# Kernel tuning notes

Hardware: AMD Instinct MI355X
Metric: run time of the kernel (lower is better)

The kernel has to match this reference:

```python
import jax, jax.numpy as jnp
import numpy as np

N_COMP = 8
N_BASIS = 16
N_FEATURES = 64
N_CAT = 8
N_CONT = 56
N_UNIQUE = 100
BATCH = 32768
T0, T1 = 0.0, 10.0
SEP = 1e-3  # constants.MIN_TRANSITION_POINT_SEP
SIGNS = np.array([1.0, -1.0, 1.0, -1.0, 1.0, -1.0, 1.0, -1.0], dtype=np.float32)
CONT_IDX = np.arange(N_CONT)
CAT_IDX = np.arange(N_CONT, N_FEATURES)


def _offset():
    # torch_inverse_softplus(avg_interval_per_feature)
    v = (T1 - T0) / N_COMP / (N_FEATURES + 1)
    return float(np.log(np.exp(v) - 1.0))


def setup_inputs():
    key = jax.random.key(0)
    ks = jax.random.split(key, 11)
    off = _offset()
    B = jax.random.normal(ks[0], (BATCH, N_CONT, N_BASIS), jnp.float32)
    codes = jax.random.randint(ks[1], (BATCH, N_CAT), 0, N_UNIQUE)
    B_cat = jax.nn.one_hot(codes, N_UNIQUE, dtype=jnp.float32).reshape(BATCH, N_CAT * N_UNIQUE)
    Wh = jax.random.normal(ks[2], (N_BASIS, N_CONT, N_COMP), jnp.float32) + off
    Wh_cat = jax.random.normal(ks[3], (N_CAT, N_UNIQUE, N_COMP), jnp.float32) + off
    bh = jax.random.normal(ks[4], (N_COMP,), jnp.float32) + off
    Wv = jax.random.normal(ks[5], (N_BASIS, N_CONT, N_COMP), jnp.float32)
    Wv_cat = jax.random.normal(ks[6], (N_CAT, N_UNIQUE, N_COMP), jnp.float32)
    bv = jax.random.normal(ks[7], (N_COMP,), jnp.float32)
    Wic = jax.random.normal(ks[8], (N_BASIS, N_CONT, 1), jnp.float32)
    Wic_cat = jax.random.normal(ks[9], (N_CAT, N_UNIQUE, 1), jnp.float32)
    bic = jax.random.normal(ks[10], (1,), jnp.float32)
    return {"B": B, "B_cat": B_cat, "Wh": Wh, "Wh_cat": Wh_cat, "bh": bh,
            "Wv": Wv, "Wv_cat": Wv_cat, "bv": bv,
            "Wic": Wic, "Wic_cat": Wic_cat, "bic": bic}


def _calculate_gams(B, B_cat, W, W_cat, bias, positive):
    # continuous: per-feature small matmul  (b,i,k) x (k,i,c) -> (b,c,i)
    cont = jnp.einsum('bik,kic->bci', B, W)
    # categorical: one-hot gather expressed as blockwise matmul  (b,f,n) x (f,n,c) -> (b,c,f)
    cat = jnp.einsum('bfn,fnc->bcf', B_cat.reshape(B.shape[0], N_CAT, N_UNIQUE), W_cat)
    c = W.shape[2]
    out = jnp.zeros((B.shape[0], c, N_FEATURES + 1), dtype=B.dtype)
    out = out.at[:, :, CONT_IDX].set(cont)
    out = out.at[:, :, CAT_IDX].set(cat)
    out = out.at[:, :, -1].set(bias[None, :])
    return jax.nn.softplus(out) if positive else out


def reference(B, B_cat, Wh, Wh_cat, bh, Wv, Wv_cat, bv, Wic, Wic_cat, bic):
    H = _calculate_gams(B, B_cat, Wh, Wh_cat, bh, True)      # (b, n_comp, n_feat+1)
    V = _calculate_gams(B, B_cat, Wv, Wv_cat, bv, True)      # (b, n_comp, n_feat+1)
    IC = _calculate_gams(B, B_cat, Wic, Wic_cat, bic, False)  # (b, 1, n_feat+1)
    b = B.shape[0]
    signs = jnp.asarray(SIGNS)
    h_sum = H.sum(-1)   # (b, n_comp) per-segment horizontal increments
    v_sum = V.sum(-1)
    sep = SEP * jnp.arange(1, N_COMP + 1, dtype=B.dtype)
    # sequential cumulative build == prefix sums over the composition axis
    t = jnp.concatenate([jnp.full((b, 1), T0, B.dtype),
                         T0 + jnp.cumsum(h_sum, axis=1) + sep], axis=1)  # (b, n_comp+1)
    x0 = IC.sum(-1)     # (b, 1)
    x = jnp.concatenate([x0, x0 + jnp.cumsum(signs * v_sum, axis=1)], axis=1)
    # bounded composition: clamp the last horizontal coordinate
    t = t.at[:, -1].set(jnp.maximum(t[:, -2] + SEP, T1))
    return jnp.stack([t, x], axis=-1)  # (b, n_comp+1, 2)
```

## Files before the change

### kernel.cpp

```cpp
#include <hip/hip_runtime.h>

#define NCOMP 8
#define NCONT 56
#define NCAT 8
#define NU 100
#define SEPC 1e-3f
#define T1F 10.0f

#define FSTRIDE 35
#define WS_NW4 2048
#define WS_BIAS_OFF 32768

typedef __fp16 f16x2 __attribute__((ext_vector_type(2)));
typedef _Float16 h2arith __attribute__((ext_vector_type(2)));

union H8 { f16x2 h2[4]; float4 f4; };

__device__ __forceinline__ float sp(float x) {
    return 0.69314718f * __builtin_amdgcn_logf(1.0f + __builtin_amdgcn_exp2f(x * 1.44269504f));
}

__device__ __forceinline__ f16x2 pkrtz(float a, float b) {
    return __builtin_amdgcn_cvt_pkrtz(a, b);
}

__device__ __forceinline__ float fdot2(f16x2 a, f16x2 b, float c) {
    return __builtin_amdgcn_fdot2(a, b, c, false);
}

__device__ __forceinline__ h2arith h2shfl_xor(h2arith v, int off) {
    int i = __builtin_bit_cast(int, v);
    i = __shfl_xor(i, off, 64);
    return __builtin_bit_cast(h2arith, i);
}

__device__ __forceinline__ void acc_cont(const float4* __restrict__ pw,
                                         float4 a0, float4 a1, float4 a2, float4 a3,
                                         float* sh, float* sw, float& ic) {
    f16x2 ba[8];
    ba[0] = pkrtz(a0.x, a0.y); ba[1] = pkrtz(a0.z, a0.w);
    ba[2] = pkrtz(a1.x, a1.y); ba[3] = pkrtz(a1.z, a1.w);
    ba[4] = pkrtz(a2.x, a2.y); ba[5] = pkrtz(a2.z, a2.w);
    ba[6] = pkrtz(a3.x, a3.y); ba[7] = pkrtz(a3.z, a3.w);
#pragma unroll
    for (int c = 0; c < NCOMP; ++c) {
        H8 u0, u1, v0, v1;
        u0.f4 = pw[2 * c];      u1.f4 = pw[2 * c + 1];
        v0.f4 = pw[16 + 2 * c]; v1.f4 = pw[17 + 2 * c];
        float hA = 0.0f, vA = 0.0f;
#pragma unroll
        for (int p = 0; p < 4; ++p) {
            hA = fdot2(ba[p], u0.h2[p], hA);
            vA = fdot2(ba[p], v0.h2[p], vA);
        }
#pragma unroll
        for (int p = 0; p < 4; ++p) {
            hA = fdot2(ba[4 + p], u1.h2[p], hA);
            vA = fdot2(ba[4 + p], v1.h2[p], vA);
        }
        sh[c] += sp(hA);
        sw[c] += sp(vA);
    }
    H8 i0, i1;
    i0.f4 = pw[32]; i1.f4 = pw[33];
    float iA = 0.0f;
#pragma unroll
    for (int p = 0; p < 4; ++p) iA = fdot2(ba[p], i0.h2[p], iA);
#pragma unroll
    for (int p = 0; p < 4; ++p) iA = fdot2(ba[4 + p], i1.h2[p], iA);
    ic += iA;
}

__global__ __launch_bounds__(512) void prep_kernel(
    const float* __restrict__ Wh, const float* __restrict__ Wv,
    const float* __restrict__ Wic, const float* __restrict__ bh,
    const float* __restrict__ bv, const float* __restrict__ bic,
    float4* __restrict__ ws)
{
    const int id = blockIdx.x * 512 + threadIdx.x;
    const int i  = id / FSTRIDE;
    const int rr = id - i * FSTRIDE;
    H8 u;
    u.f4 = make_float4(0.f, 0.f, 0.f, 0.f);
    if (i < NCONT && rr < 34) {
        if (rr < 32) {
            const int c = (rr & 15) >> 1;
            const int t = rr & 1;
            const float* W  = (rr < 16) ? Wh : Wv;
            const float* gp = W + (size_t)(8 * t) * 448 + i * 8 + c;
#pragma unroll
            for (int p = 0; p < 4; ++p)
                u.h2[p] = pkrtz(gp[(2 * p) * 448], gp[(2 * p + 1) * 448]);
        } else {
            const int t = rr - 32;
            const float* gp = Wic + (size_t)(8 * t) * 56 + i;
#pragma unroll
            for (int p = 0; p < 4; ++p)
                u.h2[p] = pkrtz(gp[(2 * p) * 56], gp[(2 * p + 1) * 56]);
        }
    }
    ws[id] = u.f4;
    if (id < NCOMP) {
        float2* b2 = (float2*)((char*)ws + WS_BIAS_OFF);
        b2[id] = make_float2(sp(bh[id]), sp(bv[id]));
    }
    if (id == NCOMP) {
        *((float*)((char*)ws + WS_BIAS_OFF + 64)) = bic[0];
    }
}

__global__ __launch_bounds__(512, 4) void tpm_kernel(
    const float* __restrict__ B, const float* __restrict__ Bcat,
    const float* __restrict__ Whc, const float* __restrict__ Wvc,
    const float* __restrict__ Wicc, const float4* __restrict__ ws,
    float* __restrict__ out)
{
    __shared__ float4 sW[WS_NW4];
    __shared__ float2 sBias[NCOMP];
    __shared__ float  sBic;
    __shared__ int    sCode[8][4][NCAT];

    const int tid  = threadIdx.x;
    const int lane = tid & 63;
    const int widx = tid >> 6;
    const int s = lane & 15;
    const int g = lane >> 4;
    const int R0 = (((blockIdx.x << 3) + widx) << 2);
    const int r = R0 + g;
    const float* browp = B + (size_t)r * 896;

    float4 cb0, cb1, cb2, cb3;
    {
        const float4* p = (const float4*)(browp + s * 16);
        cb0 = p[0]; cb1 = p[1]; cb2 = p[2]; cb3 = p[3];
    }

#pragma unroll
    for (int k = 0; k < 4; ++k) sW[tid + k * 512] = ws[tid + k * 512];
    if (tid < NCOMP) sBias[tid] = ((const float2*)((const char*)ws + WS_BIAS_OFF))[tid];
    if (tid == NCOMP) sBic = *((const float*)((const char*)ws + WS_BIAS_OFF + 64));
    __syncthreads();

    {
        const float4* pc = (const float4*)(Bcat + (size_t)R0 * 800);
#pragma unroll
        for (int it = 0; it < 13; ++it) {
            int idx = it * 64 + lane;
            if (it < 12 || idx < 800) {
                int row = idx / 200;
                int pos = idx - row * 200;
                float4 q = pc[idx];
                float n = (float)(4 * pos);
                float sc = q.x * (n + 1.0f) + q.y * (n + 2.0f) + q.z * (n + 3.0f) + q.w * (n + 4.0f);
                if (sc > 0.5f) {
                    int p = (int)sc - 1;
                    int f = p / NU;
                    sCode[widx][row][f] = p - f * NU;
                }
            }
        }
    }
    __threadfence_block();

    float4 p3a, p3b, p3c, p3d;
    float p3ic = 0.0f;
    if (s >= 8) {
        int fi = s - 8;
        int cc = sCode[widx][g][fi];
        int gA = fi * NU + cc;
        const float4* qh = (const float4*)(Whc + gA * 8);
        const float4* qv = (const float4*)(Wvc + gA * 8);
        p3a = qh[0]; p3b = qh[1]; p3c = qv[0]; p3d = qv[1];
        p3ic = Wicc[gA];
    }

    float sh[NCOMP], sw[NCOMP];
    float ic = 0.0f;
#pragma unroll
    for (int c = 0; c < NCOMP; ++c) { sh[c] = sw[c] = 0.0f; }

#pragma unroll
    for (int j = 0; j < 3; ++j) {
        float4 nb0, nb1, nb2, nb3;
        if (j < 2) {
            const float4* p = (const float4*)(browp + (s + 16 * (j + 1)) * 16);
            nb0 = p[0]; nb1 = p[1]; nb2 = p[2]; nb3 = p[3];
        } else {
            int f3 = (s < 8) ? (s + 48) : 48;
            const float4* p = (const float4*)(browp + f3 * 16);
            nb0 = p[0]; nb1 = p[1]; nb2 = p[2]; nb3 = p[3];
        }
        acc_cont(sW + (s + 16 * j) * FSTRIDE, cb0, cb1, cb2, cb3, sh, sw, ic);
        cb0 = nb0; cb1 = nb1; cb2 = nb2; cb3 = nb3;
    }

    if (s < 8) {
        acc_cont(sW + (s + 48) * FSTRIDE, cb0, cb1, cb2, cb3, sh, sw, ic);
    } else {
        sh[0] += sp(p3a.x); sh[1] += sp(p3a.y); sh[2] += sp(p3a.z); sh[3] += sp(p3a.w);
        sh[4] += sp(p3b.x); sh[5] += sp(p3b.y); sh[6] += sp(p3b.z); sh[7] += sp(p3b.w);
        sw[0] += sp(p3c.x); sw[1] += sp(p3c.y); sw[2] += sp(p3c.z); sw[3] += sp(p3c.w);
        sw[4] += sp(p3d.x); sw[5] += sp(p3d.y); sw[6] += sp(p3d.z); sw[7] += sp(p3d.w);
        ic += p3ic;
    }

    h2arith hw[NCOMP];
#pragma unroll
    for (int c = 0; c < NCOMP; ++c)
        hw[c] = __builtin_bit_cast(h2arith, pkrtz(sh[c], sw[c]));
#pragma unroll
    for (int off = 8; off >= 1; off >>= 1) {
#pragma unroll
        for (int c = 0; c < NCOMP; ++c)
            hw[c] = hw[c] + h2shfl_xor(hw[c], off);
        ic += __shfl_xor(ic, off, 64);
    }

    if (s < 9) {
        int m = (s == 8) ? 7 : s;
        float tj = SEPC * (float)s;
        float xj = ic + sBic;
#pragma unroll
        for (int c = 0; c < NCOMP; ++c) {
            float2 bb2 = sBias[c];
            if (c < m) tj += (float)hw[c][0] + bb2.x;
            if (c < s) {
                float vv = (float)hw[c][1] + bb2.y;
                xj += (c & 1) ? -vv : vv;
            }
        }
        if (s == 8) tj = fmaxf(tj, T1F);
        float2 o; o.x = tj; o.y = xj;
        ((float2*)out)[(size_t)r * 9 + s] = o;
    }
}

extern "C" void kernel_launch(void* const* d_in, const int* in_sizes, int n_in,
                              void* d_out, int out_size, void* d_ws, size_t ws_size,
                              hipStream_t stream) {
    (void)in_sizes; (void)n_in; (void)out_size; (void)ws_size;
    const float* B    = (const float*)d_in[0];
    const float* Bcat = (const float*)d_in[1];
    const float* Wh   = (const float*)d_in[2];
    const float* Whc  = (const float*)d_in[3];
    const float* bh   = (const float*)d_in[4];
    const float* Wv   = (const float*)d_in[5];
    const float* Wvc  = (const float*)d_in[6];
    const float* bv   = (const float*)d_in[7];
    const float* Wic  = (const float*)d_in[8];
    const float* Wicc = (const float*)d_in[9];
    const float* bic  = (const float*)d_in[10];
    float* out = (float*)d_out;
    float4* ws = (float4*)d_ws;

    hipLaunchKernelGGL(prep_kernel, dim3(4), dim3(512), 0, stream,
                       Wh, Wv, Wic, bh, bv, bic, ws);
    hipLaunchKernelGGL(tpm_kernel, dim3(1024), dim3(512), 0, stream,
                       B, Bcat, Whc, Wvc, Wicc, ws, out);
}
```

Measured before the change: 260.3 us.

## Read packed weights directly from global memory instead of staging in LDS

Drops the per-block copy of the 32KB packed fp16 weight table into shared memory and its barrier. The weights are re-laid out feature-major (row r, feature f) so that lanes of a wave reading consecutive features make coalesced global/L2 loads. With LDS use down to the tiny code table, the launch bound's occupancy hint is raised from 4 to 8. The cost is that every block repeatedly reads weights through the cache hierarchy instead of LDS, with higher latency per access.

Result: slower. 326.6 us (+25.4%).

```diff
diff --git a/kernel.cpp b/kernel.cpp
--- a/kernel.cpp
+++ b/kernel.cpp
@@ -7,9 +7,7 @@
 #define SEPC 1e-3f
 #define T1F 10.0f
 
-#define FSTRIDE 35
-#define WS_NW4 2048
-#define WS_BIAS_OFF 32768
+#define WS_BIAS_OFF 31744
 
 typedef __fp16 f16x2 __attribute__((ext_vector_type(2)));
 typedef _Float16 h2arith __attribute__((ext_vector_type(2)));
@@ -34,7 +32,7 @@
     return __builtin_bit_cast(h2arith, i);
 }
 
-__device__ __forceinline__ void acc_cont(const float4* __restrict__ pw,
+__device__ __forceinline__ void acc_cont(const float4* __restrict__ pwf,
                                          float4 a0, float4 a1, float4 a2, float4 a3,
                                          float* sh, float* sw, float& ic) {
     f16x2 ba[8];
@@ -45,8 +43,8 @@
 #pragma unroll
     for (int c = 0; c < NCOMP; ++c) {
         H8 u0, u1, v0, v1;
-        u0.f4 = pw[2 * c];      u1.f4 = pw[2 * c + 1];
-        v0.f4 = pw[16 + 2 * c]; v1.f4 = pw[17 + 2 * c];
+        u0.f4 = pwf[(2 * c) * NCONT];      u1.f4 = pwf[(2 * c + 1) * NCONT];
+        v0.f4 = pwf[(16 + 2 * c) * NCONT]; v1.f4 = pwf[(17 + 2 * c) * NCONT];
         float hA = 0.0f, vA = 0.0f;
 #pragma unroll
         for (int p = 0; p < 4; ++p) {
@@ -62,7 +60,7 @@
         sw[c] += sp(vA);
     }
     H8 i0, i1;
-    i0.f4 = pw[32]; i1.f4 = pw[33];
+    i0.f4 = pwf[32 * NCONT]; i1.f4 = pwf[33 * NCONT];
     float iA = 0.0f;
 #pragma unroll
     for (int p = 0; p < 4; ++p) iA = fdot2(ba[p], i0.h2[p], iA);
@@ -78,28 +76,28 @@
     float4* __restrict__ ws)
 {
     const int id = blockIdx.x * 512 + threadIdx.x;
-    const int i  = id / FSTRIDE;
-    const int rr = id - i * FSTRIDE;
-    H8 u;
-    u.f4 = make_float4(0.f, 0.f, 0.f, 0.f);
-    if (i < NCONT && rr < 34) {
-        if (rr < 32) {
-            const int c = (rr & 15) >> 1;
+    if (id < 34 * NCONT) {
+        const int r = id / NCONT;
+        const int f = id - r * NCONT;
+        H8 u;
+        if (r < 32) {
+            const int rr = r & 15;
+            const int c = rr >> 1;
             const int t = rr & 1;
-            const float* W  = (rr < 16) ? Wh : Wv;
-            const float* gp = W + (size_t)(8 * t) * 448 + i * 8 + c;
+            const float* W  = (r < 16) ? Wh : Wv;
+            const float* gp = W + (size_t)(8 * t) * 448 + f * 8 + c;
 #pragma unroll
             for (int p = 0; p < 4; ++p)
                 u.h2[p] = pkrtz(gp[(2 * p) * 448], gp[(2 * p + 1) * 448]);
         } else {
-            const int t = rr - 32;
-            const float* gp = Wic + (size_t)(8 * t) * 56 + i;
+            const int t = r - 32;
+            const float* gp = Wic + (size_t)(8 * t) * 56 + f;
 #pragma unroll
             for (int p = 0; p < 4; ++p)
                 u.h2[p] = pkrtz(gp[(2 * p) * 56], gp[(2 * p + 1) * 56]);
         }
-    }
-    ws[id] = u.f4;
+        ws[id] = u.f4;
+    }
     if (id < NCOMP) {
         float2* b2 = (float2*)((char*)ws + WS_BIAS_OFF);
         b2[id] = make_float2(sp(bh[id]), sp(bv[id]));
@@ -109,16 +107,13 @@
     }
 }
 
-__global__ __launch_bounds__(512, 4) void tpm_kernel(
+__global__ __launch_bounds__(512, 8) void tpm_kernel(
     const float* __restrict__ B, const float* __restrict__ Bcat,
     const float* __restrict__ Whc, const float* __restrict__ Wvc,
     const float* __restrict__ Wicc, const float4* __restrict__ ws,
     float* __restrict__ out)
 {
-    __shared__ float4 sW[WS_NW4];
-    __shared__ float2 sBias[NCOMP];
-    __shared__ float  sBic;
-    __shared__ int    sCode[8][4][NCAT];
+    __shared__ int sCode[8][4][NCAT];
 
     const int tid  = threadIdx.x;
     const int lane = tid & 63;
@@ -134,12 +129,6 @@
         const float4* p = (const float4*)(browp + s * 16);
         cb0 = p[0]; cb1 = p[1]; cb2 = p[2]; cb3 = p[3];
     }
-
-#pragma unroll
-    for (int k = 0; k < 4; ++k) sW[tid + k * 512] = ws[tid + k * 512];
-    if (tid < NCOMP) sBias[tid] = ((const float2*)((const char*)ws + WS_BIAS_OFF))[tid];
-    if (tid == NCOMP) sBic = *((const float*)((const char*)ws + WS_BIAS_OFF + 64));
-    __syncthreads();
 
     {
         const float4* pc = (const float4*)(Bcat + (size_t)R0 * 800);
@@ -190,12 +179,12 @@
             const float4* p = (const float4*)(browp + f3 * 16);
             nb0 = p[0]; nb1 = p[1]; nb2 = p[2]; nb3 = p[3];
         }
-        acc_cont(sW + (s + 16 * j) * FSTRIDE, cb0, cb1, cb2, cb3, sh, sw, ic);
+        acc_cont(ws + (s + 16 * j), cb0, cb1, cb2, cb3, sh, sw, ic);
         cb0 = nb0; cb1 = nb1; cb2 = nb2; cb3 = nb3;
     }
 
     if (s < 8) {
-        acc_cont(sW + (s + 48) * FSTRIDE, cb0, cb1, cb2, cb3, sh, sw, ic);
+        acc_cont(ws + (s + 48), cb0, cb1, cb2, cb3, sh, sw, ic);
     } else {
         sh[0] += sp(p3a.x); sh[1] += sp(p3a.y); sh[2] += sp(p3a.z); sh[3] += sp(p3a.w);
         sh[4] += sp(p3b.x); sh[5] += sp(p3b.y); sh[6] += sp(p3b.z); sh[7] += sp(p3b.w);
@@ -217,12 +206,14 @@
     }
 
     if (s < 9) {
+        const float2* b2 = (const float2*)((const char*)ws + WS_BIAS_OFF);
+        float bicv = *((const float*)((const char*)ws + WS_BIAS_OFF + 64));
         int m = (s == 8) ? 7 : s;
         float tj = SEPC * (float)s;
-        float xj = ic + sBic;
+        float xj = ic + bicv;
 #pragma unroll
         for (int c = 0; c < NCOMP; ++c) {
-            float2 bb2 = sBias[c];
+            float2 bb2 = b2[c];
             if (c < m) tj += (float)hw[c][0] + bb2.x;
             if (c < s) {
                 float vv = (float)hw[c][1] + bb2.y;
```

## Interleave one-hot categorical scan with continuous accumulation to overlap loads

Applied to the files above, without the earlier changes.

Splits the B_cat one-hot scan into batches of prefetched float4 loads and interleaves them with the three continuous-feature accumulation stages. Previously the whole categorical scan ran, with its own load latency, before any continuous work started. The B_cat reads now overlap with the B reads and the FMA work, at the cost of more live registers. The categorical gather is delayed until after the accumulation.

After: 594.6 us. 2.28x slower.

```diff
diff --git a/kernel.cpp b/kernel.cpp
--- a/kernel.cpp
+++ b/kernel.cpp
@@ -128,12 +128,17 @@
     const int R0 = (((blockIdx.x << 3) + widx) << 2);
     const int r = R0 + g;
     const float* browp = B + (size_t)r * 896;
+    const float4* pcat = (const float4*)(Bcat + (size_t)R0 * 800);
 
     float4 cb0, cb1, cb2, cb3;
     {
         const float4* p = (const float4*)(browp + s * 16);
         cb0 = p[0]; cb1 = p[1]; cb2 = p[2]; cb3 = p[3];
     }
+    float4 qa0 = pcat[lane];
+    float4 qa1 = pcat[64 + lane];
+    float4 qa2 = pcat[128 + lane];
+    float4 qa3 = pcat[192 + lane];
 
 #pragma unroll
     for (int k = 0; k < 4; ++k) sW[tid + k * 512] = ws[tid + k * 512];
@@ -141,25 +146,60 @@
     if (tid == NCOMP) sBic = *((const float*)((const char*)ws + WS_BIAS_OFF + 64));
     __syncthreads();
 
-    {
-        const float4* pc = (const float4*)(Bcat + (size_t)R0 * 800);
-#pragma unroll
-        for (int it = 0; it < 13; ++it) {
-            int idx = it * 64 + lane;
-            if (it < 12 || idx < 800) {
-                int row = idx / 200;
-                int pos = idx - row * 200;
-                float4 q = pc[idx];
-                float n = (float)(4 * pos);
-                float sc = q.x * (n + 1.0f) + q.y * (n + 2.0f) + q.z * (n + 3.0f) + q.w * (n + 4.0f);
-                if (sc > 0.5f) {
-                    int p = (int)sc - 1;
-                    int f = p / NU;
-                    sCode[widx][row][f] = p - f * NU;
-                }
+    auto scan1 = [&](float4 q, int it) {
+        int idx = it * 64 + lane;
+        if (it < 12 || idx < 800) {
+            int row = idx / 200;
+            int pos = idx - row * 200;
+            float n = (float)(4 * pos);
+            float sc = q.x * (n + 1.0f) + q.y * (n + 2.0f) + q.z * (n + 3.0f) + q.w * (n + 4.0f);
+            if (sc > 0.5f) {
+                int p = (int)sc - 1;
+                int f = p / NU;
+                sCode[widx][row][f] = p - f * NU;
             }
         }
-    }
+    };
+
+    float sh[NCOMP], sw[NCOMP];
+    float ic = 0.0f;
+#pragma unroll
+    for (int c = 0; c < NCOMP; ++c) { sh[c] = sw[c] = 0.0f; }
+
+    float4 nb0, nb1, nb2, nb3;
+    {
+        const float4* p = (const float4*)(browp + (s + 16) * 16);
+        nb0 = p[0]; nb1 = p[1]; nb2 = p[2]; nb3 = p[3];
+    }
+    acc_cont(sW + s * FSTRIDE, cb0, cb1, cb2, cb3, sh, sw, ic);
+    scan1(qa0, 0); scan1(qa1, 1); scan1(qa2, 2); scan1(qa3, 3);
+    qa0 = pcat[256 + lane];
+    qa1 = pcat[320 + lane];
+    qa2 = pcat[384 + lane];
+    qa3 = pcat[448 + lane];
+    float4 qa4 = pcat[512 + lane];
+    cb0 = nb0; cb1 = nb1; cb2 = nb2; cb3 = nb3;
+
+    {
+        const float4* p = (const float4*)(browp + (s + 32) * 16);
+        nb0 = p[0]; nb1 = p[1]; nb2 = p[2]; nb3 = p[3];
+    }
+    acc_cont(sW + (s + 16) * FSTRIDE, cb0, cb1, cb2, cb3, sh, sw, ic);
+    scan1(qa0, 4); scan1(qa1, 5); scan1(qa2, 6); scan1(qa3, 7); scan1(qa4, 8);
+    qa0 = pcat[576 + lane];
+    qa1 = pcat[640 + lane];
+    qa2 = pcat[704 + lane];
+    qa3 = make_float4(0.f, 0.f, 0.f, 0.f);
+    if (lane < 32) qa3 = pcat[768 + lane];
+    cb0 = nb0; cb1 = nb1; cb2 = nb2; cb3 = nb3;
+
+    {
+        int f3 = (s < 8) ? (s + 48) : 48;
+        const float4* p = (const float4*)(browp + f3 * 16);
+        nb0 = p[0]; nb1 = p[1]; nb2 = p[2]; nb3 = p[3];
+    }
+    acc_cont(sW + (s + 32) * FSTRIDE, cb0, cb1, cb2, cb3, sh, sw, ic);
+    scan1(qa0, 9); scan1(qa1, 10); scan1(qa2, 11); scan1(qa3, 12);
     __threadfence_block();
 
     float4 p3a, p3b, p3c, p3d;
@@ -173,26 +213,7 @@
         p3a = qh[0]; p3b = qh[1]; p3c = qv[0]; p3d = qv[1];
         p3ic = Wicc[gA];
     }
-
-    float sh[NCOMP], sw[NCOMP];
-    float ic = 0.0f;
-#pragma unroll
-    for (int c = 0; c < NCOMP; ++c) { sh[c] = sw[c] = 0.0f; }
-
-#pragma unroll
-    for (int j = 0; j < 3; ++j) {
-        float4 nb0, nb1, nb2, nb3;
-        if (j < 2) {
-            const float4* p = (const float4*)(browp + (s + 16 * (j + 1)) * 16);
-            nb0 = p[0]; nb1 = p[1]; nb2 = p[2]; nb3 = p[3];
-        } else {
-            int f3 = (s < 8) ? (s + 48) : 48;
-            const float4* p = (const float4*)(browp + f3 * 16);
-            nb0 = p[0]; nb1 = p[1]; nb2 = p[2]; nb3 = p[3];
-        }
-        acc_cont(sW + (s + 16 * j) * FSTRIDE, cb0, cb1, cb2, cb3, sh, sw, ic);
-        cb0 = nb0; cb1 = nb1; cb2 = nb2; cb3 = nb3;
-    }
+    cb0 = nb0; cb1 = nb1; cb2 = nb2; cb3 = nb3;
 
     if (s < 8) {
         acc_cont(sW + (s + 48) * FSTRIDE, cb0, cb1, cb2, cb3, sh, sw, ic);
```

## Split one-hot categorical scan into a separate kernel writing byte codes

Applied to the files above, without the earlier changes.

Moves the scan of the one-hot categorical matrix out of the main kernel into a dedicated scan_kernel that writes per-row byte codes to workspace. The main kernel then reads those codes directly, drops its shared-memory code table, and moves the shared weight staging and barrier after the categorical gathers. The intent is to shorten the main kernel's critical path and let it run with less memory traffic interleaved with the B stream. It adds an extra kernel launch and a small round trip through global memory for the codes, while the total bytes read from Bcat stay the same.

After: 265.5 us. About the same (+2.0%).

```diff
diff --git a/kernel.cpp b/kernel.cpp
--- a/kernel.cpp
+++ b/kernel.cpp
@@ -10,6 +10,7 @@
 #define FSTRIDE 35
 #define WS_NW4 2048
 #define WS_BIAS_OFF 32768
+#define WS_CODES_OFF 65536
 
 typedef __fp16 f16x2 __attribute__((ext_vector_type(2)));
 typedef _Float16 h2arith __attribute__((ext_vector_type(2)));
@@ -109,16 +110,39 @@
     }
 }
 
+__global__ __launch_bounds__(256, 4) void scan_kernel(
+    const float* __restrict__ Bcat, unsigned char* __restrict__ codes)
+{
+    const int t   = blockIdx.x * 256 + threadIdx.x;
+    const int row = t >> 4;
+    const int sub = t & 15;
+    const float4* pc = (const float4*)(Bcat + (size_t)row * 800);
+#pragma unroll
+    for (int k = 0; k < 13; ++k) {
+        int pos = sub + (k << 4);
+        if (pos < 200) {
+            float4 q = pc[pos];
+            float n = (float)(4 * pos);
+            float sc = q.x * (n + 1.0f) + q.y * (n + 2.0f)
+                     + q.z * (n + 3.0f) + q.w * (n + 4.0f);
+            if (sc > 0.5f) {
+                int p = (int)sc - 1;
+                int f = p / NU;
+                codes[(row << 3) + f] = (unsigned char)(p - f * NU);
+            }
+        }
+    }
+}
+
 __global__ __launch_bounds__(512, 4) void tpm_kernel(
-    const float* __restrict__ B, const float* __restrict__ Bcat,
-    const float* __restrict__ Whc, const float* __restrict__ Wvc,
-    const float* __restrict__ Wicc, const float4* __restrict__ ws,
+    const float* __restrict__ B, const float* __restrict__ Whc,
+    const float* __restrict__ Wvc, const float* __restrict__ Wicc,
+    const float4* __restrict__ ws, const unsigned char* __restrict__ codes,
     float* __restrict__ out)
 {
     __shared__ float4 sW[WS_NW4];
     __shared__ float2 sBias[NCOMP];
     __shared__ float  sBic;
-    __shared__ int    sCode[8][4][NCAT];
 
     const int tid  = threadIdx.x;
     const int lane = tid & 63;
@@ -135,44 +159,23 @@
         cb0 = p[0]; cb1 = p[1]; cb2 = p[2]; cb3 = p[3];
     }
 
-#pragma unroll
-    for (int k = 0; k < 4; ++k) sW[tid + k * 512] = ws[tid + k * 512];
-    if (tid < NCOMP) sBias[tid] = ((const float2*)((const char*)ws + WS_BIAS_OFF))[tid];
-    if (tid == NCOMP) sBic = *((const float*)((const char*)ws + WS_BIAS_OFF + 64));
-    __syncthreads();
-
-    {
-        const float4* pc = (const float4*)(Bcat + (size_t)R0 * 800);
-#pragma unroll
-        for (int it = 0; it < 13; ++it) {
-            int idx = it * 64 + lane;
-            if (it < 12 || idx < 800) {
-                int row = idx / 200;
-                int pos = idx - row * 200;
-                float4 q = pc[idx];
-                float n = (float)(4 * pos);
-                float sc = q.x * (n + 1.0f) + q.y * (n + 2.0f) + q.z * (n + 3.0f) + q.w * (n + 4.0f);
-                if (sc > 0.5f) {
-                    int p = (int)sc - 1;
-                    int f = p / NU;
-                    sCode[widx][row][f] = p - f * NU;
-                }
-            }
-        }
-    }
-    __threadfence_block();
-
     float4 p3a, p3b, p3c, p3d;
     float p3ic = 0.0f;
     if (s >= 8) {
         int fi = s - 8;
-        int cc = sCode[widx][g][fi];
+        int cc = codes[(r << 3) + fi];
         int gA = fi * NU + cc;
         const float4* qh = (const float4*)(Whc + gA * 8);
         const float4* qv = (const float4*)(Wvc + gA * 8);
         p3a = qh[0]; p3b = qh[1]; p3c = qv[0]; p3d = qv[1];
         p3ic = Wicc[gA];
     }
+
+#pragma unroll
+    for (int k = 0; k < 4; ++k) sW[tid + k * 512] = ws[tid + k * 512];
+    if (tid < NCOMP) sBias[tid] = ((const float2*)((const char*)ws + WS_BIAS_OFF))[tid];
+    if (tid == NCOMP) sBic = *((const float*)((const char*)ws + WS_BIAS_OFF + 64));
+    __syncthreads();
 
     float sh[NCOMP], sw[NCOMP];
     float ic = 0.0f;
@@ -252,9 +255,12 @@
     const float* bic  = (const float*)d_in[10];
     float* out = (float*)d_out;
     float4* ws = (float4*)d_ws;
+    unsigned char* codes = (unsigned char*)d_ws + WS_CODES_OFF;
 
     hipLaunchKernelGGL(prep_kernel, dim3(4), dim3(512), 0, stream,
                        Wh, Wv, Wic, bh, bv, bic, ws);
+    hipLaunchKernelGGL(scan_kernel, dim3(2048), dim3(256), 0, stream,
+                       Bcat, codes);
     hipLaunchKernelGGL(tpm_kernel, dim3(1024), dim3(512), 0, stream,
-                       B, Bcat, Whc, Wvc, Wicc, ws, out);
-}
+                       B, Whc, Wvc, Wicc, ws, codes, out);
+}
```
